# Performance work log

Measured on AMD Instinct MI355X. Metric: run time of the kernel, lower is better.

The kernel has to match this reference:

```python
import jax, jax.numpy as jnp
import numpy as np


def setup_inputs() -> dict:
    key = jax.random.key(0)
    B, C, T, F = 16, 2, 1000, 257
    k1, = jax.random.split(key, 1)
    inp = jax.random.normal(k1, (B, C, T, F, 2), dtype=jnp.float32)
    weights = jnp.ones((1, C, 1, F, 1), dtype=jnp.float32)   # init constant 1
    bias = jnp.zeros((1, C, 1, F, 1), dtype=jnp.float32)     # init constant 0
    alpha = jnp.full((1, C, F, 1), -4.0, dtype=jnp.float32)  # init constant -4
    s_1 = jnp.zeros((B, C, F, 1), dtype=jnp.float32)
    return {"input": inp, "weights": weights, "bias": bias, "alpha": alpha, "s_1": s_1}


def reference(input, weights, bias, alpha, s_1):
    # input: [B, C, T, F, 2]
    in_data2 = jnp.sum(input ** 2, axis=-1, keepdims=True)  # [B, C, T, F, 1]
    a = jax.nn.sigmoid(alpha)                               # [1, C, F, 1]

    def step(s, x):
        s = s * (1.0 - a) + x * a   # EMA over time, per (c, f)
        return s, s

    # scan over time axis -> move T to leading axis
    xs = jnp.moveaxis(in_data2, 2, 0)          # [T, B, C, F, 1]
    s_last, smooth = jax.lax.scan(step, s_1, xs)
    smooth = jnp.sqrt(jnp.moveaxis(smooth, 0, 2))  # [B, C, T, F, 1]

    res = input / (smooth + 1e-8) * weights + bias
    return res, s_last
```

## Files before the change

kernel.cpp:

```cpp
#include <hip/hip_runtime.h>

#define BB 16
#define CC 2
#define TT 1000
#define FF 257
#define NBC (BB * CC)
#define NCHAIN (NBC * FF)
#define RES_ELEMS ((size_t)BB * CC * TT * FF * 2)

#define TC 20
#define KC (TT / TC)
#define ROWF (FF * 2)
#define TILEF (TC * ROWF)
#define TILE4 (TILEF / 4)
#define NTHR 512
#define NBLK (NBC * KC)


__global__ __launch_bounds__(NTHR, 4) void fnorm_sums(
    const float* __restrict__ input,
    const float* __restrict__ alpha,
    float* __restrict__ e_ws)
{
    __shared__ float lds[TILEF];
    const int bc = blockIdx.x / KC;
    const int k  = blockIdx.x % KC;

    const float4* __restrict__ src =
        (const float4*)(input + (size_t)bc * (TT * ROWF) + (size_t)k * TILEF);
    for (int i = threadIdx.x; i < TILE4; i += NTHR)
        ((float4*)lds)[i] = src[i];
    __syncthreads();

    const int f = threadIdx.x;
    if (f < FF) {
        const int cf = (bc & 1) * FF + f;
        const float av = 1.0f / (1.0f + __expf(-alpha[cf]));
        const float om = 1.0f - av;
        float s = 0.0f;
        #pragma unroll
        for (int t = 0; t < TC; ++t) {
            float2 v = ((const float2*)lds)[t * FF + f];
            s = fmaf(fmaf(v.x, v.x, v.y * v.y), av, s * om);
        }
        e_ws[k * NCHAIN + bc * FF + f] = s;
    }
}

__global__ __launch_bounds__(NTHR, 4) void fnorm_apply(
    const float* __restrict__ input,
    const float* __restrict__ weights,
    const float* __restrict__ bias,
    const float* __restrict__ alpha,
    const float* __restrict__ s1,
    float* __restrict__ out,
    const float* __restrict__ e_ws)
{
    __shared__ float lds[TILEF];
    const int bc = blockIdx.x / KC;
    const int k  = blockIdx.x % KC;

    const size_t base = (size_t)bc * (TT * ROWF) + (size_t)k * TILEF;
    const float4* __restrict__ src = (const float4*)(input + base);
    for (int i = threadIdx.x; i < TILE4; i += NTHR)
        ((float4*)lds)[i] = src[i];

    const int f = threadIdx.x;
    float s = 0.0f, av = 0.0f, om = 0.0f, w = 0.0f, bi = 0.0f;
    if (f < FF) {
        const int cf = (bc & 1) * FF + f;
        av = 1.0f / (1.0f + __expf(-alpha[cf]));
        om = 1.0f - av;
        w  = weights[cf];
        bi = bias[cf];
        const float om2 = om * om, om4 = om2 * om2;
        const float om8 = om4 * om4, om16 = om8 * om8;
        const float p = om16 * om4;

        const int chain = bc * FF + f;
        s = s1[chain];
        #pragma unroll
        for (int kk = 0; kk < KC - 1; ++kk) {
            if (kk < k) s = fmaf(s, p, e_ws[kk * NCHAIN + chain]);
        }
    }
    __syncthreads();

    if (f < FF) {
        #pragma unroll
        for (int t = 0; t < TC; ++t) {
            float2 v = ((const float2*)lds)[t * FF + f];
            s = fmaf(fmaf(v.x, v.x, v.y * v.y), av, s * om);
            const float inv = __frsqrt_rn(s + 1e-16f) * w;
            float2 y;
            y.x = fmaf(v.x, inv, bi);
            y.y = fmaf(v.y, inv, bi);
            ((float2*)lds)[t * FF + f] = y;
        }
        if (k == KC - 1)
            out[RES_ELEMS + (size_t)(bc * FF + f)] = s;
    }
    __syncthreads();

    float4* __restrict__ dst = (float4*)(out + base);
    for (int i = threadIdx.x; i < TILE4; i += NTHR)
        dst[i] = ((const float4*)lds)[i];
}

extern "C" void kernel_launch(void* const* d_in, const int* in_sizes, int n_in,
                              void* d_out, int out_size, void* d_ws, size_t ws_size,
                              hipStream_t stream) {
    const float* input   = (const float*)d_in[0];
    const float* weights = (const float*)d_in[1];
    const float* bias    = (const float*)d_in[2];
    const float* alpha   = (const float*)d_in[3];
    const float* s1      = (const float*)d_in[4];
    float* out  = (float*)d_out;
    float* e_ws = (float*)d_ws;

    dim3 grid(NBLK), block(NTHR);
    hipLaunchKernelGGL(fnorm_sums,  grid, block, 0, stream, input, alpha, e_ws);
    hipLaunchKernelGGL(fnorm_apply, grid, block, 0, stream,
                       input, weights, bias, alpha, s1, out, e_ws);
}
```

Measured before the change: 147.9 us.

## Add separate prefix-scan kernel for chunk carries and halve time chunk size

```diff
diff --git a/kernel.cpp b/kernel.cpp
--- a/kernel.cpp
+++ b/kernel.cpp
@@ -8,19 +8,20 @@
 #define NCHAIN (NBC * FF)
 #define RES_ELEMS ((size_t)BB * CC * TT * FF * 2)
 
-#define TC 20
+#define TC 10
 #define KC (TT / TC)
 #define ROWF (FF * 2)
 #define TILEF (TC * ROWF)
 #define TILE4 (TILEF / 4)
-#define NTHR 512
+#define NTHR 320
 #define NBLK (NBC * KC)
+#define PBATCH 20
 
 
 __global__ __launch_bounds__(NTHR, 4) void fnorm_sums(
     const float* __restrict__ input,
     const float* __restrict__ alpha,
-    float* __restrict__ e_ws)
+    float* __restrict__ ws)
 {
     __shared__ float lds[TILEF];
     const int bc = blockIdx.x / KC;
@@ -43,8 +44,40 @@
             float2 v = ((const float2*)lds)[t * FF + f];
             s = fmaf(fmaf(v.x, v.x, v.y * v.y), av, s * om);
         }
-        e_ws[k * NCHAIN + bc * FF + f] = s;
+        ws[k * NCHAIN + bc * FF + f] = s;
     }
+}
+
+__global__ __launch_bounds__(256) void fnorm_prefix(
+    const float* __restrict__ alpha,
+    const float* __restrict__ s1,
+    float* __restrict__ out,
+    float* ws)
+{
+    const int ch = blockIdx.x * 256 + threadIdx.x;
+    if (ch >= NCHAIN) return;
+    const int f  = ch % FF;
+    const int bc = ch / FF;
+    const int cf = (bc & 1) * FF + f;
+
+    const float av = 1.0f / (1.0f + __expf(-alpha[cf]));
+    const float om = 1.0f - av;
+    const float om2 = om * om, om4 = om2 * om2, om8 = om4 * om4;
+    const float p = om8 * om2;
+
+    float S = s1[ch];
+    float e[PBATCH];
+    for (int kb = 0; kb < KC; kb += PBATCH) {
+        #pragma unroll
+        for (int j = 0; j < PBATCH; ++j)
+            e[j] = ws[(kb + j) * NCHAIN + ch];
+        #pragma unroll
+        for (int j = 0; j < PBATCH; ++j) {
+            ws[(kb + j) * NCHAIN + ch] = S;
+            S = fmaf(S, p, e[j]);
+        }
+    }
+    out[RES_ELEMS + (size_t)ch] = S;
 }
 
 __global__ __launch_bounds__(NTHR, 4) void fnorm_apply(
@@ -52,9 +85,8 @@
     const float* __restrict__ weights,
     const float* __restrict__ bias,
     const float* __restrict__ alpha,
-    const float* __restrict__ s1,
     float* __restrict__ out,
-    const float* __restrict__ e_ws)
+    const float* __restrict__ ws)
 {
     __shared__ float lds[TILEF];
     const int bc = blockIdx.x / KC;
@@ -66,23 +98,14 @@
         ((float4*)lds)[i] = src[i];
 
     const int f = threadIdx.x;
-    float s = 0.0f, av = 0.0f, om = 0.0f, w = 0.0f, bi = 0.0f;
+    float s = 0.f, av = 0.f, om = 0.f, w = 0.f, bi = 0.f;
     if (f < FF) {
         const int cf = (bc & 1) * FF + f;
         av = 1.0f / (1.0f + __expf(-alpha[cf]));
         om = 1.0f - av;
         w  = weights[cf];
         bi = bias[cf];
-        const float om2 = om * om, om4 = om2 * om2;
-        const float om8 = om4 * om4, om16 = om8 * om8;
-        const float p = om16 * om4;
-
-        const int chain = bc * FF + f;
-        s = s1[chain];
-        #pragma unroll
-        for (int kk = 0; kk < KC - 1; ++kk) {
-            if (kk < k) s = fmaf(s, p, e_ws[kk * NCHAIN + chain]);
-        }
+        s  = ws[k * NCHAIN + bc * FF + f];
     }
     __syncthreads();
 
@@ -97,8 +120,6 @@
             y.y = fmaf(v.y, inv, bi);
             ((float2*)lds)[t * FF + f] = y;
         }
-        if (k == KC - 1)
-            out[RES_ELEMS + (size_t)(bc * FF + f)] = s;
     }
     __syncthreads();
 
@@ -115,11 +136,13 @@
     const float* bias    = (const float*)d_in[2];
     const float* alpha   = (const float*)d_in[3];
     const float* s1      = (const float*)d_in[4];
-    float* out  = (float*)d_out;
-    float* e_ws = (float*)d_ws;
+    float* out = (float*)d_out;
+    float* ws  = (float*)d_ws;
 
-    dim3 grid(NBLK), block(NTHR);
-    hipLaunchKernelGGL(fnorm_sums,  grid, block, 0, stream, input, alpha, e_ws);
-    hipLaunchKernelGGL(fnorm_apply, grid, block, 0, stream,
-                       input, weights, bias, alpha, s1, out, e_ws);
+    hipLaunchKernelGGL(fnorm_sums, dim3(NBLK), dim3(NTHR), 0, stream,
+                       input, alpha, ws);
+    hipLaunchKernelGGL(fnorm_prefix, dim3((NCHAIN + 255) / 256), dim3(256), 0,
+                       stream, alpha, s1, out, ws);
+    hipLaunchKernelGGL(fnorm_apply, dim3(NBLK), dim3(NTHR), 0, stream,
+                       input, weights, bias, alpha, out, ws);
 }
```

New measurement: 137.5 us. 1.08x faster.

## Fuse two-pass EMA scan into single-pass decoupled look-back kernel

Applied to the files above, without the earlier changes.

```diff
diff --git a/kernel.cpp b/kernel.cpp
--- a/kernel.cpp
+++ b/kernel.cpp
@@ -8,85 +8,117 @@
 #define NCHAIN (NBC * FF)
 #define RES_ELEMS ((size_t)BB * CC * TT * FF * 2)
 
-#define TC 20
+#define TC 10
 #define KC (TT / TC)
 #define ROWF (FF * 2)
 #define TILEF (TC * ROWF)
 #define TILE4 (TILEF / 4)
-#define NTHR 512
+#define NTHR 320
 #define NBLK (NBC * KC)
+#define STATE_WORDS (KC * NCHAIN)
+#define STATE_BYTES ((size_t)STATE_WORDS * 4)
 
 
-__global__ __launch_bounds__(NTHR, 4) void fnorm_sums(
-    const float* __restrict__ input,
-    const float* __restrict__ alpha,
-    float* __restrict__ e_ws)
-{
-    __shared__ float lds[TILEF];
-    const int bc = blockIdx.x / KC;
-    const int k  = blockIdx.x % KC;
-
-    const float4* __restrict__ src =
-        (const float4*)(input + (size_t)bc * (TT * ROWF) + (size_t)k * TILEF);
-    for (int i = threadIdx.x; i < TILE4; i += NTHR)
-        ((float4*)lds)[i] = src[i];
-    __syncthreads();
-
-    const int f = threadIdx.x;
-    if (f < FF) {
-        const int cf = (bc & 1) * FF + f;
-        const float av = 1.0f / (1.0f + __expf(-alpha[cf]));
-        const float om = 1.0f - av;
-        float s = 0.0f;
-        #pragma unroll
-        for (int t = 0; t < TC; ++t) {
-            float2 v = ((const float2*)lds)[t * FF + f];
-            s = fmaf(fmaf(v.x, v.x, v.y * v.y), av, s * om);
-        }
-        e_ws[k * NCHAIN + bc * FF + f] = s;
-    }
+__device__ __forceinline__ unsigned pk(unsigned st, float v) {
+    return (__float_as_uint(v) & ~3u) | st;
 }
 
-__global__ __launch_bounds__(NTHR, 4) void fnorm_apply(
+__global__ __launch_bounds__(NTHR, 8) void fnorm_fused(
     const float* __restrict__ input,
     const float* __restrict__ weights,
     const float* __restrict__ bias,
     const float* __restrict__ alpha,
     const float* __restrict__ s1,
     float* __restrict__ out,
-    const float* __restrict__ e_ws)
+    unsigned* __restrict__ state,
+    unsigned* __restrict__ vcnt)
 {
     __shared__ float lds[TILEF];
-    const int bc = blockIdx.x / KC;
-    const int k  = blockIdx.x % KC;
+    __shared__ unsigned sh_rank;
+
+    if (threadIdx.x == 0)
+        sh_rank = __hip_atomic_fetch_add(vcnt, 1u, __ATOMIC_RELAXED,
+                                         __HIP_MEMORY_SCOPE_AGENT);
+    __syncthreads();
+    const int r  = (int)sh_rank;
+    const int bc = r & (NBC - 1);
+    const int k  = r >> 5;
 
     const size_t base = (size_t)bc * (TT * ROWF) + (size_t)k * TILEF;
     const float4* __restrict__ src = (const float4*)(input + base);
     for (int i = threadIdx.x; i < TILE4; i += NTHR)
         ((float4*)lds)[i] = src[i];
+    __syncthreads();
 
     const int f = threadIdx.x;
-    float s = 0.0f, av = 0.0f, om = 0.0f, w = 0.0f, bi = 0.0f;
+    const int chain = bc * FF + f;
+    float av = 0.f, om = 0.f, w = 0.f, bi = 0.f, e = 0.f, p10 = 0.f;
     if (f < FF) {
         const int cf = (bc & 1) * FF + f;
         av = 1.0f / (1.0f + __expf(-alpha[cf]));
         om = 1.0f - av;
         w  = weights[cf];
         bi = bias[cf];
-        const float om2 = om * om, om4 = om2 * om2;
-        const float om8 = om4 * om4, om16 = om8 * om8;
-        const float p = om16 * om4;
+        float s = 0.f;
+        #pragma unroll
+        for (int t = 0; t < TC; ++t) {
+            float2 v = ((const float2*)lds)[t * FF + f];
+            s = fmaf(fmaf(v.x, v.x, v.y * v.y), av, s * om);
+        }
+        e = s;
+        const float om2 = om * om, om4 = om2 * om2, om8 = om4 * om4;
+        p10 = om8 * om2;
+    }
 
-        const int chain = bc * FF + f;
-        s = s1[chain];
-        #pragma unroll
-        for (int kk = 0; kk < KC - 1; ++kk) {
-            if (kk < k) s = fmaf(s, p, e_ws[kk * NCHAIN + chain]);
+    float S = 0.f;
+    if (k == 0) {
+        if (f < FF) {
+            S = s1[chain];
+            __hip_atomic_store(&state[chain], pk(2u, fmaf(S, p10, e)),
+                               __ATOMIC_RELAXED, __HIP_MEMORY_SCOPE_AGENT);
         }
+    } else if (f < FF) {
+        if (k < KC - 1)
+            __hip_atomic_store(&state[k * NCHAIN + chain], pk(1u, e),
+                               __ATOMIC_RELAXED, __HIP_MEMORY_SCOPE_AGENT);
+        float E = 0.f, P = 1.f;
+        int j = k - 1;
+        bool done = false;
+        while (!done) {
+            unsigned wv[4];
+            const int nb = (j + 1 < 4) ? (j + 1) : 4;
+            #pragma unroll
+            for (int l = 0; l < 4; ++l)
+                if (l < nb)
+                    wv[l] = __hip_atomic_load(&state[(j - l) * NCHAIN + chain],
+                                              __ATOMIC_RELAXED,
+                                              __HIP_MEMORY_SCOPE_AGENT);
+            #pragma unroll
+            for (int l = 0; l < 4; ++l) {
+                if (l < nb && !done) {
+                    unsigned v = wv[l];
+                    while ((v & 3u) == 0u) {
+                        __builtin_amdgcn_s_sleep(1);
+                        v = __hip_atomic_load(&state[(j - l) * NCHAIN + chain],
+                                              __ATOMIC_RELAXED,
+                                              __HIP_MEMORY_SCOPE_AGENT);
+                    }
+                    E = fmaf(P, __uint_as_float(v & ~3u), E);
+                    if ((v & 3u) == 2u) done = true;
+                    else                P *= p10;
+                }
+            }
+            j -= nb;
+            if (j < 0) done = true;
+        }
+        S = E;
+        if (k < KC - 1)
+            __hip_atomic_store(&state[k * NCHAIN + chain], pk(2u, fmaf(S, p10, e)),
+                               __ATOMIC_RELAXED, __HIP_MEMORY_SCOPE_AGENT);
     }
-    __syncthreads();
 
     if (f < FF) {
+        float s = S;
         #pragma unroll
         for (int t = 0; t < TC; ++t) {
             float2 v = ((const float2*)lds)[t * FF + f];
@@ -98,7 +130,7 @@
             ((float2*)lds)[t * FF + f] = y;
         }
         if (k == KC - 1)
-            out[RES_ELEMS + (size_t)(bc * FF + f)] = s;
+            out[RES_ELEMS + (size_t)chain] = s;
     }
     __syncthreads();
 
@@ -115,11 +147,12 @@
     const float* bias    = (const float*)d_in[2];
     const float* alpha   = (const float*)d_in[3];
     const float* s1      = (const float*)d_in[4];
-    float* out  = (float*)d_out;
-    float* e_ws = (float*)d_ws;
+    float* out = (float*)d_out;
 
-    dim3 grid(NBLK), block(NTHR);
-    hipLaunchKernelGGL(fnorm_sums,  grid, block, 0, stream, input, alpha, e_ws);
-    hipLaunchKernelGGL(fnorm_apply, grid, block, 0, stream,
-                       input, weights, bias, alpha, s1, out, e_ws);
+    unsigned* state = (unsigned*)d_ws;
+    unsigned* vcnt  = (unsigned*)((char*)d_ws + STATE_BYTES);
+
+    hipMemsetAsync(d_ws, 0, STATE_BYTES + 8, stream);
+    hipLaunchKernelGGL(fnorm_fused, dim3(NBLK), dim3(NTHR), 0, stream,
+                       input, weights, bias, alpha, s1, out, state, vcnt);
 }
```

Result: slower. 158.3 us (+7.0%).
